# Optimization experiments

Measured on AMD Instinct MI355X. Metric: run time of the kernel, lower is better.

## Reference

```python
import jax, jax.numpy as jnp
import numpy as np

D = 512      # embed_dim
H = 8        # num_heads
B = 32       # number of graphs
L = 512      # max graph size (padded length)
DEG = 8      # avg out-degree
NUM_GIN = 3  # StructureExtractor num_layers


def setup_inputs() -> dict:
    key = jax.random.key(0)
    ks = jax.random.split(key, 24)

    # ragged graph sizes 256..504, ptr is the CSR boundary vector
    sizes = 256 + 8 * np.arange(B)
    ptr_np = np.concatenate([[0], np.cumsum(sizes)]).astype(np.int64)
    N = int(ptr_np[-1])  # 12160 total nodes

    rng = np.random.RandomState(0)
    node_graph = np.repeat(np.arange(B), sizes)
    offs = ptr_np[node_graph]
    sz = sizes[node_graph]
    # DEG random in-graph neighbors per node
    dst = (rng.random((N, DEG)) * sz[:, None]).astype(np.int64) + offs[:, None]
    src = np.repeat(np.arange(N, dtype=np.int64), DEG)
    edge_index = jnp.asarray(np.stack([src, dst.ravel()]), dtype=jnp.int64)

    # DAG reachability mask: True = masked. Keep key 0 open so no row is fully -inf.
    md = rng.random((B, L, L)) > 0.5
    md[:, :, 0] = False
    mask_dag_ = jnp.asarray(md)

    def lin(k, fan_in, fan_out):
        return jax.random.normal(k, (fan_in, fan_out), jnp.float32) / np.sqrt(fan_in)

    inp = {
        "x": jax.random.normal(ks[0], (N, D), jnp.float32),
        "edge_index": edge_index,
        "mask_dag_": mask_dag_,
        "ptr": jnp.asarray(ptr_np),
        # GIN layers: MLP(Linear(D,D) -> ReLU -> Linear(D,D)) per layer
        "gin_w1": jnp.stack([lin(ks[1 + i], D, D) for i in range(NUM_GIN)]),
        "gin_b1": jnp.zeros((NUM_GIN, D), jnp.float32),
        "gin_w2": jnp.stack([lin(ks[4 + i], D, D) for i in range(NUM_GIN)]),
        "gin_b2": jnp.zeros((NUM_GIN, D), jnp.float32),
        "bn_gamma": jnp.ones((D,), jnp.float32),
        "bn_beta": jnp.zeros((D,), jnp.float32),
        "se_out_w": lin(ks[7], D, D),
        "se_out_b": jnp.zeros((D,), jnp.float32),
        "qk_w": lin(ks[8], D, 2 * D),
        "qk_b": jnp.zeros((2 * D,), jnp.float32),
        "v_w": lin(ks[9], D, D),
        "v_b": jnp.zeros((D,), jnp.float32),
        "out_w": lin(ks[10], D, D),
        "out_b": jnp.zeros((D,), jnp.float32),
    }
    return inp


def reference(x, edge_index, mask_dag_, ptr,
              gin_w1, gin_b1, gin_w2, gin_b2,
              bn_gamma, bn_beta, se_out_w, se_out_b,
              qk_w, qk_b, v_w, v_b, out_w, out_b):
    N = x.shape[0]
    nb = ptr.shape[0] - 1
    Lm = mask_dag_.shape[1]
    hd = D // H
    scale = hd ** -0.5

    # v = to_v(x)
    v = x @ v_w + v_b

    # StructureExtractor: 3 GIN layers (eps=0) + BatchNorm (batch stats) + Linear
    src, dst = edge_index[0], edge_index[1]
    h = x
    for i in range(NUM_GIN):
        agg = jax.ops.segment_sum(h[src], dst, num_segments=N)
        z = h + agg                                  # (1+eps)*x + sum neighbors, eps=0
        z = jax.nn.relu(z @ gin_w1[i] + gin_b1[i]) @ gin_w2[i] + gin_b2[i]
        h = jax.nn.relu(z)
    mean = h.mean(axis=0)
    var = h.var(axis=0)
    h = (h - mean) / jnp.sqrt(var + 1e-5) * bn_gamma + bn_beta
    x_struct = h @ se_out_w + se_out_b

    # qk = to_qk(x_struct).chunk(2): k = first half, q = second half (original order)
    qk = x_struct @ qk_w + qk_b
    k_flat, q_flat = jnp.split(qk, 2, axis=-1)

    # pad ragged batch to [B, L, D]
    node_ar = jnp.arange(N)
    bi = jnp.searchsorted(ptr, node_ar, side='right') - 1   # graph id per node
    pos = node_ar - ptr[bi]                                 # in-graph position
    sizes = ptr[1:] - ptr[:-1]

    def pad(t):
        return jnp.zeros((nb, Lm, t.shape[-1]), t.dtype).at[bi, pos].set(t)

    def heads(t):  # [B, L, D] -> [B, H, L, hd]
        return t.reshape(nb, Lm, H, hd).transpose(0, 2, 1, 3)

    q = heads(pad(q_flat))
    k = heads(pad(k_flat))
    vp = heads(pad(v))

    dots = jnp.einsum('bhid,bhjd->bhij', q, k) * scale
    pad_mask = jnp.arange(Lm)[None, :] >= sizes[:, None]     # True = padded key
    dots = jnp.where(pad_mask[:, None, None, :], -jnp.inf, dots)
    dots = jnp.where(mask_dag_[:, None, :, :], -jnp.inf, dots)
    attn = jax.nn.softmax(dots, axis=-1)

    out = jnp.einsum('bhij,bhjd->bhid', attn, vp)            # [B, H, L, hd]
    out = out.transpose(0, 2, 1, 3).reshape(nb, Lm, D)[bi, pos]  # unpad -> [N, D]
    return out @ out_w + out_b
```

## Files before the change

### kernel.cpp

```cpp
#include <hip/hip_runtime.h>
#include <hip/hip_bf16.h>
#include <cstdint>
#include <cstddef>

#define D 512
#define NHEAD 8
#define LMAX 512
#define NGIN 3

typedef unsigned short u16;
typedef unsigned long long u64;
typedef __attribute__((ext_vector_type(8))) short short8;
typedef __attribute__((ext_vector_type(8))) unsigned short ushort8;
typedef __attribute__((ext_vector_type(4))) unsigned short us4;
typedef __attribute__((ext_vector_type(4))) float f32x4;

static __device__ inline u16 f2bf(float f){
    union { float f; uint32_t u; } c; c.f = f;
    uint32_t r = (c.u + 0x7fffu + ((c.u >> 16) & 1u)) >> 16;
    return (u16)r;
}
static __device__ inline u16 tbf(float f){
    union { float f; uint32_t u; } c; c.f = f;
    return (u16)(c.u >> 16);
}
static __device__ inline float bf2f(u16 h){
    union { uint32_t u; float f; } c; c.u = ((uint32_t)h) << 16; return c.f;
}

#define GLOAD_LDS16(SRC, DST) \
    __builtin_amdgcn_global_load_lds( \
        (const __attribute__((address_space(1))) void*)(SRC), \
        (__attribute__((address_space(3))) void*)(DST), 16, 0, 0)

__global__ void probe_kernel(const int* __restrict__ ptr_raw,
                             const unsigned char* __restrict__ mask_raw,
                             int* __restrict__ flags){
    if (threadIdx.x == 0){
        flags[0] = (ptr_raw[1] == 0) ? 1 : 0;
        int cntOdd = 0, cnt4 = 0;
        for (int i = 1; i < 2048; i += 2) cntOdd += (mask_raw[i] != 0);
        for (int i = 4; i < 2048; i += 8) cnt4   += (mask_raw[i] != 0);
        flags[1] = (cntOdd > 64) ? 1 : ((cnt4 > 16) ? 4 : 8);
    }
}

__global__ void conv_int_kernel(const int* __restrict__ raw, int* __restrict__ outp,
                                const int* __restrict__ flags, int n){
    int i = blockIdx.x*256 + threadIdx.x;
    if (i < n) outp[i] = flags[0] ? raw[2*i] : raw[i];
}

__global__ void maskbits_kernel(const unsigned char* __restrict__ raw,
                                u64* __restrict__ outp,
                                const int* __restrict__ flags, int total){
    int idx = blockIdx.x*256 + threadIdx.x;
    if (idx >= total) return;
    int w = flags[1];
    size_t ebase = (size_t)(idx >> 3) * 512 + (size_t)(idx & 7) * 64;
    u64 bits = 0;
    if (w == 1){
        const u64* p8 = (const u64*)(raw + ebase);
        #pragma unroll
        for (int g = 0; g < 8; g++){
            u64 v = p8[g];
            #pragma unroll
            for (int by = 0; by < 8; by++)
                if ((v >> (by*8)) & 0xffull) bits |= 1ull << (g*8 + by);
        }
    } else {
        for (int j = 0; j < 64; j++)
            if (raw[(ebase + j) * (size_t)w]) bits |= 1ull << j;
    }
    outp[idx] = bits;
}

__global__ void count_kernel(const int* __restrict__ ei, int* __restrict__ deg, int E, int N){
    int e = blockIdx.x*256 + threadIdx.x;
    if (e < E){
        int d = ei[E + e];
        if ((unsigned)d < (unsigned)N) atomicAdd(&deg[d], 1);
    }
}

__global__ void scan_kernel(const int* __restrict__ deg, int* __restrict__ offs, int n){
    __shared__ int wsum[16];
    __shared__ int carry_s;
    int tid = threadIdx.x, lane = tid & 63, wv = tid >> 6;
    if (tid == 0){ carry_s = 0; offs[0] = 0; }
    __syncthreads();
    int nChunks = (n + 1023) / 1024;
    for (int ch = 0; ch < nChunks; ch++){
        int i = ch*1024 + tid;
        int val = (i < n) ? deg[i] : 0;
        int s = val;
        #pragma unroll
        for (int off = 1; off < 64; off <<= 1){
            int t = __shfl_up(s, off);
            if (lane >= off) s += t;
        }
        if (lane == 63) wsum[wv] = s;
        __syncthreads();
        if (wv == 0){
            int t = (lane < 16) ? wsum[lane] : 0;
            #pragma unroll
            for (int off = 1; off < 16; off <<= 1){
                int u = __shfl_up(t, off);
                if (lane >= off) t += u;
            }
            if (lane < 16) wsum[lane] = t;
        }
        __syncthreads();
        int wbase = wv ? wsum[wv-1] : 0;
        if (i < n) offs[i+1] = carry_s + wbase + s;
        __syncthreads();
        if (tid == 1023) carry_s += wsum[15];
        __syncthreads();
    }
}

__global__ void fill_kernel(const int* __restrict__ ei, const int* __restrict__ offs,
                            int* __restrict__ cursor, int* __restrict__ in_src, int E, int N){
    int e = blockIdx.x*256 + threadIdx.x;
    if (e < E){
        int d = ei[E + e];
        if ((unsigned)d < (unsigned)N){
            int slot = atomicAdd(&cursor[d], 1);
            in_src[offs[d] + slot] = ei[e];
        }
    }
}

__global__ void split_kernel(const float* __restrict__ in, u16* __restrict__ hi,
                             u16* __restrict__ lo, int total4){
    int i = blockIdx.x*256 + threadIdx.x;
    if (i >= total4) return;
    float4 v = *(const float4*)(in + (size_t)i*4);
    float fv[4] = {v.x, v.y, v.z, v.w};
    us4 h4, l4;
    #pragma unroll
    for (int j = 0; j < 4; j++){
        u16 hh = tbf(fv[j]);
        h4[j] = hh;
        l4[j] = tbf(fv[j] - bf2f(hh));
    }
    *(us4*)(hi + (size_t)i*4) = h4;
    *(us4*)(lo + (size_t)i*4) = l4;
}

__global__ __launch_bounds__(256) void gather_kernel(const u16* __restrict__ hh,
        const u16* __restrict__ hl,
        const int* __restrict__ offs, const int* __restrict__ in_src,
        u16* __restrict__ oh, u16* __restrict__ ol, int N){
    int node = blockIdx.x*2 + (threadIdx.x >> 7);
    if (node >= N) return;
    int t = threadIdx.x & 127;
    size_t rb = (size_t)node*D + t*4;
    us4 vh = *(const us4*)(hh + rb);
    us4 vl = *(const us4*)(hl + rb);
    float a[4];
    #pragma unroll
    for (int j = 0; j < 4; j++) a[j] = bf2f(vh[j]) + bf2f(vl[j]);
    int s = offs[node], e = offs[node+1];
    for (int i = s; i < e; i++){
        size_t sb = (size_t)in_src[i]*D + t*4;
        us4 nh = *(const us4*)(hh + sb);
        us4 nl = *(const us4*)(hl + sb);
        #pragma unroll
        for (int j = 0; j < 4; j++) a[j] += bf2f(nh[j]) + bf2f(nl[j]);
    }
    us4 h4, l4;
    #pragma unroll
    for (int j = 0; j < 4; j++){
        u16 hh2 = tbf(a[j]);
        h4[j] = hh2;
        l4[j] = tbf(a[j] - bf2f(hh2));
    }
    *(us4*)(oh + rb) = h4;
    *(us4*)(ol + rb) = l4;
}

__global__ __launch_bounds__(256) void transpose_all(
        const float* __restrict__ v_w, const float* __restrict__ gin_w1,
        const float* __restrict__ gin_w2, const float* __restrict__ se_w,
        const float* __restrict__ out_w, const float* __restrict__ qk_w,
        u16* __restrict__ wtsh, u16* __restrict__ wtsl){
    const size_t SLOT = 262144;
    int z = blockIdx.z;
    int Nout = (z == 9) ? 1024 : 512;
    if (z < 9 && blockIdx.x >= 16) return;
    const float* W; int slot;
    switch (z){
        case 0: W = v_w; slot = 0; break;
        case 1: W = gin_w1;               slot = 1; break;
        case 2: W = gin_w2;               slot = 2; break;
        case 3: W = gin_w1 + 262144;      slot = 3; break;
        case 4: W = gin_w2 + 262144;      slot = 4; break;
        case 5: W = gin_w1 + 524288;      slot = 5; break;
        case 6: W = gin_w2 + 524288;      slot = 6; break;
        case 7: W = se_w;  slot = 7; break;
        case 8: W = out_w; slot = 10; break;
        default: W = qk_w; slot = 8; break;
    }
    u16* Wh = wtsh + SLOT*slot;
    u16* Wl = wtsl + SLOT*slot;
    __shared__ float T[32][33];
    int nb = blockIdx.x*32, kb = blockIdx.y*32;
    int ln = threadIdx.x & 31, lk = threadIdx.x >> 5;
    #pragma unroll
    for (int i = 0; i < 4; i++)
        T[lk + 8*i][ln] = W[(size_t)(kb + lk + 8*i)*Nout + nb + ln];
    __syncthreads();
    #pragma unroll
    for (int i = 0; i < 4; i++){
        float val = T[ln][lk + 8*i];
        u16 h = tbf(val);
        size_t idx = (size_t)(nb + lk + 8*i)*512 + kb + ln;
        Wh[idx] = h;
        Wl[idx] = tbf(val - bf2f(h));
    }
}

__global__ __launch_bounds__(256) void fold_transpose(const float* __restrict__ M1,
        const float* __restrict__ sc, u16* __restrict__ Wh, u16* __restrict__ Wl){
    __shared__ float T[32][33];
    int nb = blockIdx.x*32, kb = blockIdx.y*32;
    int ln = threadIdx.x & 31, lk = threadIdx.x >> 5;
    #pragma unroll
    for (int i = 0; i < 4; i++){
        int k = kb + lk + 8*i;
        T[lk + 8*i][ln] = M1[(size_t)k*1024 + nb + ln] * sc[k];
    }
    __syncthreads();
    #pragma unroll
    for (int i = 0; i < 4; i++){
        float val = T[ln][lk + 8*i];
        u16 h = tbf(val);
        size_t idx = (size_t)(nb + lk + 8*i)*512 + kb + ln;
        Wh[idx] = h;
        Wl[idx] = tbf(val - bf2f(h));
    }
}

__global__ void bias_fold(const float* __restrict__ M1, const float* __restrict__ sc,
        const float* __restrict__ se_b, const float* __restrict__ qk_w,
        const float* __restrict__ qk_b, float* __restrict__ bbig){
    int n = blockIdx.x;
    int lane = threadIdx.x;
    float acc = 0.f;
    for (int k = lane; k < 512; k += 64)
        acc += sc[512+k]*M1[(size_t)k*1024 + n] + se_b[k]*qk_w[(size_t)k*1024 + n];
    #pragma unroll
    for (int off = 32; off > 0; off >>= 1) acc += __shfl_xor(acc, off);
    if (lane == 0) bbig[n] = acc + qk_b[n];
}

template<int ACT, int EPI>
__global__ __launch_bounds__(256) void gemm_ps(const u16* __restrict__ Ahg,
        const u16* __restrict__ Alg,
        const u16* __restrict__ Wth, const u16* __restrict__ Wtl,
        const float* __restrict__ bias,
        void* __restrict__ C0, void* __restrict__ C1, int K, int Nout){
    __shared__ __align__(16) u16 Ah[128][64];
    __shared__ __align__(16) u16 Al[128][64];
    __shared__ __align__(16) u16 Bh[64][64];
    __shared__ __align__(16) u16 Bl[64][64];
    int tid = threadIdx.x;
    int gx = gridDim.x;
    int nwg = gx * gridDim.y;
    int orig = blockIdx.x + gx*blockIdx.y;
    int q8 = nwg >> 3, r8 = nwg & 7;
    int xcd = orig & 7, pos = orig >> 3;
    int wg = (xcd < r8 ? xcd*(q8+1) : r8*(q8+1) + (xcd - r8)*q8) + pos;
    int rowBase = (wg / gx) * 128, colBase = (wg % gx) * 64;
    int w = tid >> 6, l = tid & 63, lg = l >> 4, lm = l & 15;
    int wr = w >> 1, wc = w & 1;
    f32x4 acc[4][2] = {};
    const u16* Ahp = Ahg + (size_t)rowBase*K;
    const u16* Alp = Alg + (size_t)rowBase*K;
    const u16* Wph = Wth + (size_t)colBase*K;
    const u16* Wpl = Wtl + (size_t)colBase*K;
    int srowA[4], scolA[4], srowB[2], scolB[2];
    #pragma unroll
    for (int c = 0; c < 4; c++){
        int slot = c*256 + tid;
        srowA[c] = slot >> 3;
        scolA[c] = ((slot & 7) ^ (srowA[c] & 7)) * 8;
    }
    #pragma unroll
    for (int c = 0; c < 2; c++){
        int slot = c*256 + tid;
        srowB[c] = slot >> 3;
        scolB[c] = ((slot & 7) ^ (srowB[c] & 7)) * 8;
    }
    for (int k0 = 0; k0 < K; k0 += 64){
        #pragma unroll
        for (int c = 0; c < 4; c++){
            int slot = c*256 + tid;
            size_t so = (size_t)srowA[c]*K + k0 + scolA[c];
            GLOAD_LDS16(Ahp + so, &Ah[0][0] + slot*8);
            GLOAD_LDS16(Alp + so, &Al[0][0] + slot*8);
        }
        #pragma unroll
        for (int c = 0; c < 2; c++){
            int slot = c*256 + tid;
            size_t so = (size_t)srowB[c]*K + k0 + scolB[c];
            GLOAD_LDS16(Wph + so, &Bh[0][0] + slot*8);
            GLOAD_LDS16(Wpl + so, &Bl[0][0] + slot*8);
        }
        __syncthreads();
        #pragma unroll
        for (int ks = 0; ks < 2; ks++){
            int scg = ((ks*4 + lg) ^ (lm & 7)) * 8;
            short8 ah[4], al[4], bh[2], bl[2];
            #pragma unroll
            for (int mf = 0; mf < 4; mf++){
                ah[mf] = *(const short8*)&Ah[wr*64 + mf*16 + lm][scg];
                al[mf] = *(const short8*)&Al[wr*64 + mf*16 + lm][scg];
            }
            #pragma unroll
            for (int nf = 0; nf < 2; nf++){
                bh[nf] = *(const short8*)&Bh[wc*32 + nf*16 + lm][scg];
                bl[nf] = *(const short8*)&Bl[wc*32 + nf*16 + lm][scg];
            }
            __builtin_amdgcn_s_setprio(1);
            #pragma unroll
            for (int mf = 0; mf < 4; mf++)
                #pragma unroll
                for (int nf = 0; nf < 2; nf++){
                    acc[mf][nf] = __builtin_amdgcn_mfma_f32_16x16x32_bf16(ah[mf], bh[nf], acc[mf][nf], 0, 0, 0);
                    acc[mf][nf] = __builtin_amdgcn_mfma_f32_16x16x32_bf16(al[mf], bh[nf], acc[mf][nf], 0, 0, 0);
                    acc[mf][nf] = __builtin_amdgcn_mfma_f32_16x16x32_bf16(ah[mf], bl[nf], acc[mf][nf], 0, 0, 0);
                }
            __builtin_amdgcn_s_setprio(0);
        }
        __syncthreads();
    }
    #pragma unroll
    for (int nf = 0; nf < 2; nf++){
        int col = colBase + wc*32 + nf*16 + lm;
        float bv = bias[col];
        #pragma unroll
        for (int mf = 0; mf < 4; mf++){
            int row = rowBase + wr*64 + mf*16 + lg*4;
            #pragma unroll
            for (int j = 0; j < 4; j++){
                float o = acc[mf][nf][j] + bv;
                if (ACT) o = fmaxf(o, 0.f);
                size_t idx = (size_t)(row + j)*Nout + col;
                if (EPI == 0){
                    ((float*)C0)[idx] = o;
                } else if (EPI == 1){
                    u16 hh = tbf(o);
                    ((u16*)C0)[idx] = hh;
                    ((u16*)C1)[idx] = tbf(o - bf2f(hh));
                } else {
                    ((u16*)C0)[idx] = f2bf(o);
                }
            }
        }
    }
}

__global__ __launch_bounds__(256) void bn_stats_kernel(const u16* __restrict__ Ah,
        const u16* __restrict__ Al, float* __restrict__ sums, int n){
    int c = threadIdx.x;
    int r0 = blockIdx.x*128, r1 = min(n, r0+128);
    float s0=0.f, s1=0.f, q0=0.f, q1=0.f;
    for (int r = r0; r < r1; r++){
        float v0 = bf2f(Ah[(size_t)r*D + c])       + bf2f(Al[(size_t)r*D + c]);
        float v1 = bf2f(Ah[(size_t)r*D + 256 + c]) + bf2f(Al[(size_t)r*D + 256 + c]);
        s0 += v0; q0 += v0*v0; s1 += v1; q1 += v1*v1;
    }
    atomicAdd(&sums[c], s0);
    atomicAdd(&sums[c+256], s1);
    atomicAdd(&sums[512+c], q0);
    atomicAdd(&sums[512+c+256], q1);
}

__global__ void bn_final_kernel(const float* __restrict__ sums, const float* __restrict__ gamma,
        const float* __restrict__ beta, float* __restrict__ sc, int n){
    int c = threadIdx.x;
    float mean = sums[c] / (float)n;
    float var = sums[512+c] / (float)n - mean*mean;
    float r = rsqrtf(var + 1e-5f);
    float scale = r * gamma[c];
    sc[c] = scale;
    sc[512+c] = beta[c] - mean*scale;
}

#define ATS 72
__global__ __launch_bounds__(512) void attn_mfma_kernel(const u16* __restrict__ qkH,
        const u16* __restrict__ qkL, const u16* __restrict__ vbf,
        const u64* __restrict__ maskbits,
        const int* __restrict__ ptr, u16* __restrict__ oh, u16* __restrict__ ol, int N){
    __shared__ u16 Kh[64][ATS];
    __shared__ u16 Kl[64][ATS];
    __shared__ u16 Vt[64][ATS];
    __shared__ u16 Pl[8][16][ATS];
    int b = blockIdx.z, h = blockIdx.y;
    int base = ptr[b], size = ptr[b+1] - base;
    int q0 = blockIdx.x * 128;
    if (q0 >= size) return;
    int tid = threadIdx.x, w = tid >> 6, l = tid & 63;
    int lg = l >> 4, lm = l & 15;
    short8 qh[2], ql[2];
    {
        int qrow = q0 + w*16 + lm;
        int qr = (qrow < size) ? qrow : 0;
        const u16* qph = qkH + (size_t)(base + qr)*1024 + 512 + h*64;
        const u16* qpl = qkL + (size_t)(base + qr)*1024 + 512 + h*64;
        #pragma unroll
        for (int ks = 0; ks < 2; ks++){
            short8 th = *(const short8*)(qph + ks*32 + lg*8);
            short8 tl = *(const short8*)(qpl + ks*32 + lg*8);
            if (qrow >= size){ th = short8{0,0,0,0,0,0,0,0}; tl = short8{0,0,0,0,0,0,0,0}; }
            qh[ks] = th; ql[ks] = tl;
        }
    }
    f32x4 acco[4] = {};
    float mrow[4], lrow[4];
    #pragma unroll
    for (int j = 0; j < 4; j++){ mrow[j] = -INFINITY; lrow[j] = 0.f; }
    int nt = (size + 63) >> 6;
    for (int t = 0; t < nt; t++){
        int j0 = t*64;
        __syncthreads();
        {
            int jj = tid & 63, db = (tid >> 6)*8;
            int key = j0 + jj;
            bool ok = key < size;
            size_t node = (size_t)(base + (ok ? key : 0));
            const u16* khp = qkH + node*1024 + h*64 + db;
            const u16* klp = qkL + node*1024 + h*64 + db;
            const u16* vp  = vbf + node*512  + h*64 + db;
            ushort8 z = {0,0,0,0,0,0,0,0};
            ushort8 kh0 = ok ? *(const ushort8*)(khp) : z;
            ushort8 kl0 = ok ? *(const ushort8*)(klp) : z;
            ushort8 v0  = ok ? *(const ushort8*)(vp)  : z;
            *(ushort8*)&Kh[jj][db] = kh0;
            *(ushort8*)&Kl[jj][db] = kl0;
            #pragma unroll
            for (int i = 0; i < 8; i++) Vt[db + i][jj] = v0[i];
        }
        __syncthreads();
        f32x4 sc[4] = {};
        __builtin_amdgcn_s_setprio(1);
        #pragma unroll
        for (int nf = 0; nf < 4; nf++)
            #pragma unroll
            for (int ks = 0; ks < 2; ks++){
                short8 kh = *(const short8*)&Kh[nf*16 + lm][ks*32 + lg*8];
                short8 kl = *(const short8*)&Kl[nf*16 + lm][ks*32 + lg*8];
                sc[nf] = __builtin_amdgcn_mfma_f32_16x16x32_bf16(qh[ks], kh, sc[nf], 0, 0, 0);
                sc[nf] = __builtin_amdgcn_mfma_f32_16x16x32_bf16(ql[ks], kh, sc[nf], 0, 0, 0);
                sc[nf] = __builtin_amdgcn_mfma_f32_16x16x32_bf16(qh[ks], kl, sc[nf], 0, 0, 0);
            }
        __builtin_amdgcn_s_setprio(0);
        u64 mb[4];
        #pragma unroll
        for (int j = 0; j < 4; j++)
            mb[j] = maskbits[((size_t)b*LMAX + (q0 + w*16 + lg*4 + j))*8 + t];
        float mx[4], alpha[4];
        #pragma unroll
        for (int j = 0; j < 4; j++){
            float s0 = -INFINITY;
            #pragma unroll
            for (int nf = 0; nf < 4; nf++){
                int key = j0 + nf*16 + lm;
                float s = sc[nf][j] * 0.125f;
                bool msk = (key >= size) || ((mb[j] >> (nf*16 + lm)) & 1);
                s = msk ? -INFINITY : s;
                sc[nf][j] = s;
                s0 = fmaxf(s0, s);
            }
            #pragma unroll
            for (int off = 1; off < 16; off <<= 1) s0 = fmaxf(s0, __shfl_xor(s0, off));
            mx[j] = s0;
        }
        #pragma unroll
        for (int j = 0; j < 4; j++){
            if (mx[j] == -INFINITY){ alpha[j] = 1.f; }
            else {
                float mn = fmaxf(mrow[j], mx[j]);
                alpha[j] = __expf(mrow[j] - mn);
                mrow[j] = mn;
            }
        }
        float ps[4] = {0.f, 0.f, 0.f, 0.f};
        #pragma unroll
        for (int nf = 0; nf < 4; nf++)
            #pragma unroll
            for (int j = 0; j < 4; j++){
                float p = (mx[j] == -INFINITY) ? 0.f : __expf(sc[nf][j] - mrow[j]);
                ps[j] += p;
                Pl[w][lg*4 + j][nf*16 + lm] = tbf(p);
            }
        #pragma unroll
        for (int j = 0; j < 4; j++){
            float s = ps[j];
            #pragma unroll
            for (int off = 1; off < 16; off <<= 1) s += __shfl_xor(s, off);
            lrow[j] = lrow[j]*alpha[j] + s;
        }
        #pragma unroll
        for (int df = 0; df < 4; df++)
            #pragma unroll
            for (int j = 0; j < 4; j++) acco[df][j] *= alpha[j];
        __builtin_amdgcn_s_setprio(1);
        #pragma unroll
        for (int ks = 0; ks < 2; ks++){
            short8 pf = *(const short8*)&Pl[w][lm][ks*32 + lg*8];
            #pragma unroll
            for (int df = 0; df < 4; df++){
                short8 vf = *(const short8*)&Vt[df*16 + lm][ks*32 + lg*8];
                acco[df] = __builtin_amdgcn_mfma_f32_16x16x32_bf16(pf, vf, acco[df], 0, 0, 0);
            }
        }
        __builtin_amdgcn_s_setprio(0);
    }
    #pragma unroll
    for (int j = 0; j < 4; j++){
        int r = q0 + w*16 + lg*4 + j;
        if (r < size){
            float inv = 1.f / lrow[j];
            #pragma unroll
            for (int df = 0; df < 4; df++){
                float o = acco[df][j] * inv;
                size_t idx = (size_t)(base + r)*D + h*64 + df*16 + lm;
                u16 hh = tbf(o);
                oh[idx] = hh;
                ol[idx] = tbf(o - bf2f(hh));
            }
        }
    }
}

extern "C" void kernel_launch(void* const* d_in, const int* in_sizes, int n_in,
                              void* d_out, int out_size, void* d_ws, size_t ws_size,
                              hipStream_t stream){
    const float* x        = (const float*)d_in[0];
    const int*   ei_raw   = (const int*)d_in[1];
    const unsigned char* mask_raw = (const unsigned char*)d_in[2];
    const int*   ptr_raw  = (const int*)d_in[3];
    const float* gin_w1   = (const float*)d_in[4];
    const float* gin_b1   = (const float*)d_in[5];
    const float* gin_w2   = (const float*)d_in[6];
    const float* gin_b2   = (const float*)d_in[7];
    const float* bn_gamma = (const float*)d_in[8];
    const float* bn_beta  = (const float*)d_in[9];
    const float* se_w     = (const float*)d_in[10];
    const float* se_b     = (const float*)d_in[11];
    const float* qk_w     = (const float*)d_in[12];
    const float* qk_b     = (const float*)d_in[13];
    const float* v_w      = (const float*)d_in[14];
    const float* v_b      = (const float*)d_in[15];
    const float* out_w    = (const float*)d_in[16];
    const float* out_b    = (const float*)d_in[17];

    const int N  = in_sizes[0] / D;
    const int E  = in_sizes[1] / 2;
    const int B  = in_sizes[3] - 1;
    const int Mn = in_sizes[2];

    char* ws = (char*)d_ws;
    char* p = ws;
    auto alloc = [&](size_t bytes) -> char* {
        char* q = p; p += (bytes + 255) & ~(size_t)255; return q;
    };
    size_t PLANE = (size_t)N * D * sizeof(u16);
    u16* pairX = (u16*)alloc(2*PLANE);
    u16* pairG = (u16*)alloc(2*PLANE);
    u16* pairT = (u16*)alloc(2*PLANE);
    u16* pairH = (u16*)alloc(2*PLANE);
    u16* v_bf  = (u16*)alloc(PLANE);
    u16* Xh = pairX, *Xl = pairX + (size_t)N*D;
    u16* Gh = pairG, *Gl = pairG + (size_t)N*D;
    u16* Th = pairT, *Tl = pairT + (size_t)N*D;
    u16* Hh = pairH, *Hl = pairH + (size_t)N*D;
    float* sums   = (float*)alloc(1024*sizeof(float));
    float* sc     = (float*)alloc(1024*sizeof(float));
    int*   flags  = (int*)alloc(16*sizeof(int));
    int*   deg    = (int*)alloc((size_t)N*sizeof(int));
    int*   offs   = (int*)alloc((size_t)(N+1)*sizeof(int));
    int*   cursor = (int*)alloc((size_t)N*sizeof(int));
    int*   in_src = (int*)alloc((size_t)E*sizeof(int));
    int*   ptr32  = (int*)alloc(64*sizeof(int));
    int*   ei32   = (int*)alloc((size_t)2*E*sizeof(int));
    u64*   mbits  = (u64*)alloc((size_t)(Mn/64)*sizeof(u64));
    u16*   wtsh   = (u16*)alloc((size_t)2883584*sizeof(u16));
    u16*   wtsl   = (u16*)alloc((size_t)2883584*sizeof(u16));
    u16*   sewh   = (u16*)alloc((size_t)D*D*sizeof(u16));
    u16*   sewl   = (u16*)alloc((size_t)D*D*sizeof(u16));
    float* M1     = (float*)alloc((size_t)D*1024*sizeof(float));
    u16*   wbig_h = (u16*)alloc((size_t)1024*D*sizeof(u16));
    u16*   wbig_l = (u16*)alloc((size_t)1024*D*sizeof(u16));
    float* bbig   = (float*)alloc(1024*sizeof(float));
    float* zbias  = (float*)alloc(1024*sizeof(float));
    const size_t SLOT = 262144;
    u16 *wh_v = wtsh, *wl_v = wtsl;
    u16 *wh_g[6], *wl_g[6];
    for (int i = 0; i < 6; i++){ wh_g[i] = wtsh + SLOT*(1+i); wl_g[i] = wtsl + SLOT*(1+i); }
    u16 *wh_qk  = wtsh + SLOT*8,  *wl_qk  = wtsl + SLOT*8;
    u16 *wh_out = wtsh + SLOT*10, *wl_out = wtsl + SLOT*10;

    probe_kernel<<<1, 64, 0, stream>>>(ptr_raw, mask_raw, flags);
    conv_int_kernel<<<1, 64, 0, stream>>>(ptr_raw, ptr32, flags, B + 1);
    conv_int_kernel<<<(2*E + 255)/256, 256, 0, stream>>>(ei_raw, ei32, flags, 2*E);
    maskbits_kernel<<<(Mn/64 + 255)/256, 256, 0, stream>>>(mask_raw, mbits, flags, Mn/64);

    hipMemsetAsync(deg, 0, (size_t)N*sizeof(int), stream);
    hipMemsetAsync(cursor, 0, (size_t)N*sizeof(int), stream);
    hipMemsetAsync(zbias, 0, 1024*sizeof(float), stream);
    count_kernel<<<(E+255)/256, 256, 0, stream>>>(ei32, deg, E, N);
    scan_kernel<<<1, 1024, 0, stream>>>(deg, offs, N);
    fill_kernel<<<(E+255)/256, 256, 0, stream>>>(ei32, offs, cursor, in_src, E, N);

    transpose_all<<<dim3(32,16,10), 256, 0, stream>>>(v_w, gin_w1, gin_w2, se_w, out_w, qk_w, wtsh, wtsl);
    split_kernel<<<(N*D/4 + 255)/256, 256, 0, stream>>>(x, Xh, Xl, N*D/4);
    split_kernel<<<(D*D/4 + 255)/256, 256, 0, stream>>>(se_w, sewh, sewl, D*D/4);

    gemm_ps<0,0><<<dim3(16,4), 256, 0, stream>>>(sewh, sewl, wh_qk, wl_qk, zbias, M1, nullptr, D, 2*D);

    dim3 g512(8, N/128), g1024(16, N/128);

    gemm_ps<0,2><<<g512, 256, 0, stream>>>(Xh, Xl, wh_v, wl_v, v_b, v_bf, nullptr, D, D);

    for (int i = 0; i < NGIN; i++){
        const u16* sh = (i == 0) ? Xh : Hh;
        const u16* sl = (i == 0) ? Xl : Hl;
        gather_kernel<<<(N+1)/2, 256, 0, stream>>>(sh, sl, offs, in_src, Gh, Gl, N);
        gemm_ps<1,1><<<g512, 256, 0, stream>>>(Gh, Gl, wh_g[2*i],   wl_g[2*i],   gin_b1 + (size_t)i*D, Th, Tl, D, D);
        gemm_ps<1,1><<<g512, 256, 0, stream>>>(Th, Tl, wh_g[2*i+1], wl_g[2*i+1], gin_b2 + (size_t)i*D, Hh, Hl, D, D);
    }

    hipMemsetAsync(sums, 0, 1024*sizeof(float), stream);
    bn_stats_kernel<<<(N+127)/128, 256, 0, stream>>>(Hh, Hl, sums, N);
    bn_final_kernel<<<1, 512, 0, stream>>>(sums, bn_gamma, bn_beta, sc, N);

    fold_transpose<<<dim3(32,16), 256, 0, stream>>>(M1, sc, wbig_h, wbig_l);
    bias_fold<<<1024, 64, 0, stream>>>(M1, sc, se_b, qk_w, qk_b, bbig);

    gemm_ps<0,1><<<g1024, 256, 0, stream>>>(Hh, Hl, wbig_h, wbig_l, bbig, pairX, pairG, D, 2*D);

    attn_mfma_kernel<<<dim3(LMAX/128, NHEAD, B), 512, 0, stream>>>(pairX, pairG, v_bf, mbits, ptr32, Th, Tl, N);

    gemm_ps<0,0><<<g512, 256, 0, stream>>>(Th, Tl, wh_out, wl_out, out_b, (float*)d_out, nullptr, D, D);
}
```

Before: 575.4 us.

## Fuse prologue kernels, merge BN fold, and drop low-order terms in two GEMMs

Folds the int conversion, mask bitpacking, weight transposes, input splits and degree counting into one multi-role launch, and reads the raw edge index directly so the int32 copy goes away. BN finalisation is merged into the weight/bias fold kernel. The V projection and the output projection now use a two-term split-bf16 GEMM with no A low part, and attention writes only a single bf16 output. This trims launches, memory traffic and MFMA work, at the cost of lower precision in those two GEMMs.

```diff
diff --git a/kernel.cpp b/kernel.cpp
--- a/kernel.cpp
+++ b/kernel.cpp
@@ -45,41 +45,113 @@
     }
 }
 
-__global__ void conv_int_kernel(const int* __restrict__ raw, int* __restrict__ outp,
-                                const int* __restrict__ flags, int n){
-    int i = blockIdx.x*256 + threadIdx.x;
-    if (i < n) outp[i] = flags[0] ? raw[2*i] : raw[i];
-}
-
-__global__ void maskbits_kernel(const unsigned char* __restrict__ raw,
-                                u64* __restrict__ outp,
-                                const int* __restrict__ flags, int total){
-    int idx = blockIdx.x*256 + threadIdx.x;
-    if (idx >= total) return;
-    int w = flags[1];
-    size_t ebase = (size_t)(idx >> 3) * 512 + (size_t)(idx & 7) * 64;
-    u64 bits = 0;
-    if (w == 1){
-        const u64* p8 = (const u64*)(raw + ebase);
-        #pragma unroll
-        for (int g = 0; g < 8; g++){
-            u64 v = p8[g];
-            #pragma unroll
-            for (int by = 0; by < 8; by++)
-                if ((v >> (by*8)) & 0xffull) bits |= 1ull << (g*8 + by);
-        }
+__global__ __launch_bounds__(256) void mega_prologue(
+        const float* __restrict__ v_w, const float* __restrict__ gin_w1,
+        const float* __restrict__ gin_w2, const float* __restrict__ se_w,
+        const float* __restrict__ out_w, const float* __restrict__ qk_w,
+        u16* __restrict__ wtsh, u16* __restrict__ wtsl,
+        const unsigned char* __restrict__ mask_raw, u64* __restrict__ mbits,
+        const float* __restrict__ x, u16* __restrict__ Xh, u16* __restrict__ Xl,
+        u16* __restrict__ sewh, u16* __restrict__ sewl,
+        const int* __restrict__ ptr_raw, int* __restrict__ ptr32,
+        const int* __restrict__ ei_raw, int* __restrict__ deg,
+        const int* __restrict__ flags,
+        int Nnodes, int E, int B, int Mn64){
+    int z = blockIdx.z;
+    int bid = blockIdx.y*32 + blockIdx.x;
+    int tid = threadIdx.x;
+    if (z <= 9){
+        int Nout = (z == 9) ? 1024 : 512;
+        if (z < 9 && blockIdx.x >= 16) return;
+        const size_t SLOT = 262144;
+        const float* W; int slot;
+        switch (z){
+            case 0: W = v_w; slot = 0; break;
+            case 1: W = gin_w1;          slot = 1; break;
+            case 2: W = gin_w2;          slot = 2; break;
+            case 3: W = gin_w1 + 262144; slot = 3; break;
+            case 4: W = gin_w2 + 262144; slot = 4; break;
+            case 5: W = gin_w1 + 524288; slot = 5; break;
+            case 6: W = gin_w2 + 524288; slot = 6; break;
+            case 7: W = se_w;  slot = 7; break;
+            case 8: W = out_w; slot = 10; break;
+            default: W = qk_w; slot = 8; break;
+        }
+        u16* Wh = wtsh + SLOT*slot;
+        u16* Wl = wtsl + SLOT*slot;
+        __shared__ float T[32][33];
+        int nb = blockIdx.x*32, kb = blockIdx.y*32;
+        int ln = tid & 31, lk = tid >> 5;
+        #pragma unroll
+        for (int i = 0; i < 4; i++)
+            T[lk + 8*i][ln] = W[(size_t)(kb + lk + 8*i)*Nout + nb + ln];
+        __syncthreads();
+        #pragma unroll
+        for (int i = 0; i < 4; i++){
+            float val = T[ln][lk + 8*i];
+            u16 h = tbf(val);
+            size_t idx = (size_t)(nb + lk + 8*i)*512 + kb + ln;
+            Wh[idx] = h;
+            Wl[idx] = tbf(val - bf2f(h));
+        }
+    } else if (z == 10){
+        int idx = bid*256 + tid;
+        if (idx >= Mn64) return;
+        int w = flags[1];
+        size_t ebase = (size_t)(idx >> 3) * 512 + (size_t)(idx & 7) * 64;
+        u64 bits = 0;
+        if (w == 1){
+            const u64* p8 = (const u64*)(mask_raw + ebase);
+            #pragma unroll
+            for (int g = 0; g < 8; g++){
+                u64 v = p8[g];
+                #pragma unroll
+                for (int by = 0; by < 8; by++)
+                    if ((v >> (by*8)) & 0xffull) bits |= 1ull << (g*8 + by);
+            }
+        } else {
+            for (int j = 0; j < 64; j++)
+                if (mask_raw[(ebase + j) * (size_t)w]) bits |= 1ull << j;
+        }
+        mbits[idx] = bits;
+    } else if (z == 11){
+        int total4 = Nnodes*D/4;
+        for (int i = bid*256 + tid; i < total4; i += 131072){
+            float4 v = *(const float4*)(x + (size_t)i*4);
+            float fv[4] = {v.x, v.y, v.z, v.w};
+            us4 h4, l4;
+            #pragma unroll
+            for (int j = 0; j < 4; j++){
+                u16 hh = tbf(fv[j]);
+                h4[j] = hh;
+                l4[j] = tbf(fv[j] - bf2f(hh));
+            }
+            *(us4*)(Xh + (size_t)i*4) = h4;
+            *(us4*)(Xl + (size_t)i*4) = l4;
+        }
+    } else if (z == 12){
+        int i = bid*256 + tid;
+        if (i >= D*D/4) return;
+        float4 v = *(const float4*)(se_w + (size_t)i*4);
+        float fv[4] = {v.x, v.y, v.z, v.w};
+        us4 h4, l4;
+        #pragma unroll
+        for (int j = 0; j < 4; j++){
+            u16 hh = tbf(fv[j]);
+            h4[j] = hh;
+            l4[j] = tbf(fv[j] - bf2f(hh));
+        }
+        *(us4*)(sewh + (size_t)i*4) = h4;
+        *(us4*)(sewl + (size_t)i*4) = l4;
+    } else if (z == 13){
+        if (bid == 0 && tid <= B)
+            ptr32[tid] = flags[0] ? ptr_raw[2*tid] : ptr_raw[tid];
     } else {
-        for (int j = 0; j < 64; j++)
-            if (raw[(ebase + j) * (size_t)w]) bits |= 1ull << j;
-    }
-    outp[idx] = bits;
-}
-
-__global__ void count_kernel(const int* __restrict__ ei, int* __restrict__ deg, int E, int N){
-    int e = blockIdx.x*256 + threadIdx.x;
-    if (e < E){
-        int d = ei[E + e];
-        if ((unsigned)d < (unsigned)N) atomicAdd(&deg[d], 1);
+        int e = bid*256 + tid;
+        if (e < E){
+            int d = flags[0] ? ei_raw[2*(E + e)] : ei_raw[E + e];
+            if ((unsigned)d < (unsigned)Nnodes) atomicAdd(&deg[d], 1);
+        }
     }
 }
 
@@ -119,33 +191,17 @@
     }
 }
 
-__global__ void fill_kernel(const int* __restrict__ ei, const int* __restrict__ offs,
-                            int* __restrict__ cursor, int* __restrict__ in_src, int E, int N){
+__global__ void fill_kernel(const int* __restrict__ ei_raw, const int* __restrict__ offs,
+                            int* __restrict__ cursor, int* __restrict__ in_src,
+                            const int* __restrict__ flags, int E, int N){
     int e = blockIdx.x*256 + threadIdx.x;
     if (e < E){
-        int d = ei[E + e];
+        int d = flags[0] ? ei_raw[2*(E + e)] : ei_raw[E + e];
         if ((unsigned)d < (unsigned)N){
             int slot = atomicAdd(&cursor[d], 1);
-            in_src[offs[d] + slot] = ei[e];
-        }
-    }
-}
-
-__global__ void split_kernel(const float* __restrict__ in, u16* __restrict__ hi,
-                             u16* __restrict__ lo, int total4){
-    int i = blockIdx.x*256 + threadIdx.x;
-    if (i >= total4) return;
-    float4 v = *(const float4*)(in + (size_t)i*4);
-    float fv[4] = {v.x, v.y, v.z, v.w};
-    us4 h4, l4;
-    #pragma unroll
-    for (int j = 0; j < 4; j++){
-        u16 hh = tbf(fv[j]);
-        h4[j] = hh;
-        l4[j] = tbf(fv[j] - bf2f(hh));
-    }
-    *(us4*)(hi + (size_t)i*4) = h4;
-    *(us4*)(lo + (size_t)i*4) = l4;
+            in_src[offs[d] + slot] = flags[0] ? ei_raw[2*e] : ei_raw[e];
+        }
+    }
 }
 
 __global__ __launch_bounds__(256) void gather_kernel(const u16* __restrict__ hh,
@@ -180,89 +236,60 @@
     *(us4*)(ol + rb) = l4;
 }
 
-__global__ __launch_bounds__(256) void transpose_all(
-        const float* __restrict__ v_w, const float* __restrict__ gin_w1,
-        const float* __restrict__ gin_w2, const float* __restrict__ se_w,
-        const float* __restrict__ out_w, const float* __restrict__ qk_w,
-        u16* __restrict__ wtsh, u16* __restrict__ wtsl){
-    const size_t SLOT = 262144;
-    int z = blockIdx.z;
-    int Nout = (z == 9) ? 1024 : 512;
-    if (z < 9 && blockIdx.x >= 16) return;
-    const float* W; int slot;
-    switch (z){
-        case 0: W = v_w; slot = 0; break;
-        case 1: W = gin_w1;               slot = 1; break;
-        case 2: W = gin_w2;               slot = 2; break;
-        case 3: W = gin_w1 + 262144;      slot = 3; break;
-        case 4: W = gin_w2 + 262144;      slot = 4; break;
-        case 5: W = gin_w1 + 524288;      slot = 5; break;
-        case 6: W = gin_w2 + 524288;      slot = 6; break;
-        case 7: W = se_w;  slot = 7; break;
-        case 8: W = out_w; slot = 10; break;
-        default: W = qk_w; slot = 8; break;
-    }
-    u16* Wh = wtsh + SLOT*slot;
-    u16* Wl = wtsl + SLOT*slot;
-    __shared__ float T[32][33];
-    int nb = blockIdx.x*32, kb = blockIdx.y*32;
-    int ln = threadIdx.x & 31, lk = threadIdx.x >> 5;
-    #pragma unroll
-    for (int i = 0; i < 4; i++)
-        T[lk + 8*i][ln] = W[(size_t)(kb + lk + 8*i)*Nout + nb + ln];
-    __syncthreads();
-    #pragma unroll
-    for (int i = 0; i < 4; i++){
-        float val = T[ln][lk + 8*i];
-        u16 h = tbf(val);
-        size_t idx = (size_t)(nb + lk + 8*i)*512 + kb + ln;
-        Wh[idx] = h;
-        Wl[idx] = tbf(val - bf2f(h));
-    }
-}
-
-__global__ __launch_bounds__(256) void fold_transpose(const float* __restrict__ M1,
-        const float* __restrict__ sc, u16* __restrict__ Wh, u16* __restrict__ Wl){
-    __shared__ float T[32][33];
-    int nb = blockIdx.x*32, kb = blockIdx.y*32;
-    int ln = threadIdx.x & 31, lk = threadIdx.x >> 5;
-    #pragma unroll
-    for (int i = 0; i < 4; i++){
-        int k = kb + lk + 8*i;
-        T[lk + 8*i][ln] = M1[(size_t)k*1024 + nb + ln] * sc[k];
-    }
-    __syncthreads();
-    #pragma unroll
-    for (int i = 0; i < 4; i++){
-        float val = T[ln][lk + 8*i];
-        u16 h = tbf(val);
-        size_t idx = (size_t)(nb + lk + 8*i)*512 + kb + ln;
-        Wh[idx] = h;
-        Wl[idx] = tbf(val - bf2f(h));
-    }
-}
-
-__global__ void bias_fold(const float* __restrict__ M1, const float* __restrict__ sc,
+__global__ __launch_bounds__(256) void fold_mega(const float* __restrict__ M1,
+        const float* __restrict__ sums, const float* __restrict__ gamma,
+        const float* __restrict__ beta,
         const float* __restrict__ se_b, const float* __restrict__ qk_w,
-        const float* __restrict__ qk_b, float* __restrict__ bbig){
-    int n = blockIdx.x;
-    int lane = threadIdx.x;
-    float acc = 0.f;
-    for (int k = lane; k < 512; k += 64)
-        acc += sc[512+k]*M1[(size_t)k*1024 + n] + se_b[k]*qk_w[(size_t)k*1024 + n];
-    #pragma unroll
-    for (int off = 32; off > 0; off >>= 1) acc += __shfl_xor(acc, off);
-    if (lane == 0) bbig[n] = acc + qk_b[n];
-}
-
-template<int ACT, int EPI>
+        const float* __restrict__ qk_b,
+        u16* __restrict__ Wh, u16* __restrict__ Wl, float* __restrict__ bbig, int n){
+    float inv_n = 1.f / (float)n;
+    if (blockIdx.z == 0){
+        __shared__ float T[32][33];
+        int nb = blockIdx.x*32, kb = blockIdx.y*32;
+        int ln = threadIdx.x & 31, lk = threadIdx.x >> 5;
+        #pragma unroll
+        for (int i = 0; i < 4; i++){
+            int k = kb + lk + 8*i;
+            float mean = sums[k] * inv_n;
+            float var = sums[512+k] * inv_n - mean*mean;
+            float scale = rsqrtf(var + 1e-5f) * gamma[k];
+            T[lk + 8*i][ln] = M1[(size_t)k*1024 + nb + ln] * scale;
+        }
+        __syncthreads();
+        #pragma unroll
+        for (int i = 0; i < 4; i++){
+            float val = T[ln][lk + 8*i];
+            u16 h = tbf(val);
+            size_t idx = (size_t)(nb + lk + 8*i)*512 + kb + ln;
+            Wh[idx] = h;
+            Wl[idx] = tbf(val - bf2f(h));
+        }
+    } else {
+        int wv = threadIdx.x >> 6, lane = threadIdx.x & 63;
+        if (wv >= 2) return;
+        int nidx = (blockIdx.y*32 + blockIdx.x)*2 + wv;
+        float acc = 0.f;
+        for (int k = lane; k < 512; k += 64){
+            float mean = sums[k] * inv_n;
+            float var = sums[512+k] * inv_n - mean*mean;
+            float scale = rsqrtf(var + 1e-5f) * gamma[k];
+            float shift = beta[k] - mean*scale;
+            acc += shift*M1[(size_t)k*1024 + nidx] + se_b[k]*qk_w[(size_t)k*1024 + nidx];
+        }
+        #pragma unroll
+        for (int off = 32; off > 0; off >>= 1) acc += __shfl_xor(acc, off);
+        if (lane == 0) bbig[nidx] = acc + qk_b[nidx];
+    }
+}
+
+template<int ACT, int EPI, int TERMS>
 __global__ __launch_bounds__(256) void gemm_ps(const u16* __restrict__ Ahg,
         const u16* __restrict__ Alg,
         const u16* __restrict__ Wth, const u16* __restrict__ Wtl,
         const float* __restrict__ bias,
         void* __restrict__ C0, void* __restrict__ C1, int K, int Nout){
     __shared__ __align__(16) u16 Ah[128][64];
-    __shared__ __align__(16) u16 Al[128][64];
+    __shared__ __align__(16) u16 Al[TERMS == 3 ? 128 : 1][64];
     __shared__ __align__(16) u16 Bh[64][64];
     __shared__ __align__(16) u16 Bl[64][64];
     int tid = threadIdx.x;
@@ -277,7 +304,7 @@
     int wr = w >> 1, wc = w & 1;
     f32x4 acc[4][2] = {};
     const u16* Ahp = Ahg + (size_t)rowBase*K;
-    const u16* Alp = Alg + (size_t)rowBase*K;
+    const u16* Alp = (TERMS == 3) ? Alg + (size_t)rowBase*K : nullptr;
     const u16* Wph = Wth + (size_t)colBase*K;
     const u16* Wpl = Wtl + (size_t)colBase*K;
     int srowA[4], scolA[4], srowB[2], scolB[2];
@@ -299,7 +326,7 @@
             int slot = c*256 + tid;
             size_t so = (size_t)srowA[c]*K + k0 + scolA[c];
             GLOAD_LDS16(Ahp + so, &Ah[0][0] + slot*8);
-            GLOAD_LDS16(Alp + so, &Al[0][0] + slot*8);
+            if (TERMS == 3) GLOAD_LDS16(Alp + so, &Al[0][0] + slot*8);
         }
         #pragma unroll
         for (int c = 0; c < 2; c++){
@@ -316,7 +343,7 @@
             #pragma unroll
             for (int mf = 0; mf < 4; mf++){
                 ah[mf] = *(const short8*)&Ah[wr*64 + mf*16 + lm][scg];
-                al[mf] = *(const short8*)&Al[wr*64 + mf*16 + lm][scg];
+                if (TERMS == 3) al[mf] = *(const short8*)&Al[wr*64 + mf*16 + lm][scg];
             }
             #pragma unroll
             for (int nf = 0; nf < 2; nf++){
@@ -329,7 +356,8 @@
                 #pragma unroll
                 for (int nf = 0; nf < 2; nf++){
                     acc[mf][nf] = __builtin_amdgcn_mfma_f32_16x16x32_bf16(ah[mf], bh[nf], acc[mf][nf], 0, 0, 0);
-                    acc[mf][nf] = __builtin_amdgcn_mfma_f32_16x16x32_bf16(al[mf], bh[nf], acc[mf][nf], 0, 0, 0);
+                    if (TERMS == 3)
+                        acc[mf][nf] = __builtin_amdgcn_mfma_f32_16x16x32_bf16(al[mf], bh[nf], acc[mf][nf], 0, 0, 0);
                     acc[mf][nf] = __builtin_amdgcn_mfma_f32_16x16x32_bf16(ah[mf], bl[nf], acc[mf][nf], 0, 0, 0);
                 }
             __builtin_amdgcn_s_setprio(0);
@@ -378,22 +406,11 @@
     atomicAdd(&sums[512+c+256], q1);
 }
 
-__global__ void bn_final_kernel(const float* __restrict__ sums, const float* __restrict__ gamma,
-        const float* __restrict__ beta, float* __restrict__ sc, int n){
-    int c = threadIdx.x;
-    float mean = sums[c] / (float)n;
-    float var = sums[512+c] / (float)n - mean*mean;
-    float r = rsqrtf(var + 1e-5f);
-    float scale = r * gamma[c];
-    sc[c] = scale;
-    sc[512+c] = beta[c] - mean*scale;
-}
-
 #define ATS 72
 __global__ __launch_bounds__(512) void attn_mfma_kernel(const u16* __restrict__ qkH,
         const u16* __restrict__ qkL, const u16* __restrict__ vbf,
         const u64* __restrict__ maskbits,
-        const int* __restrict__ ptr, u16* __restrict__ oh, u16* __restrict__ ol, int N){
+        const int* __restrict__ ptr, u16* __restrict__ oh, int N){
     __shared__ u16 Kh[64][ATS];
     __shared__ u16 Kl[64][ATS];
     __shared__ u16 Vt[64][ATS];
@@ -527,10 +544,7 @@
             #pragma unroll
             for (int df = 0; df < 4; df++){
                 float o = acco[df][j] * inv;
-                size_t idx = (size_t)(base + r)*D + h*64 + df*16 + lm;
-                u16 hh = tbf(o);
-                oh[idx] = hh;
-                ol[idx] = tbf(o - bf2f(hh));
+                oh[(size_t)(base + r)*D + h*64 + df*16 + lm] = f2bf(o);
             }
         }
     }
@@ -579,14 +593,12 @@
     u16* Th = pairT, *Tl = pairT + (size_t)N*D;
     u16* Hh = pairH, *Hl = pairH + (size_t)N*D;
     float* sums   = (float*)alloc(1024*sizeof(float));
-    float* sc     = (float*)alloc(1024*sizeof(float));
     int*   flags  = (int*)alloc(16*sizeof(int));
     int*   deg    = (int*)alloc((size_t)N*sizeof(int));
     int*   offs   = (int*)alloc((size_t)(N+1)*sizeof(int));
     int*   cursor = (int*)alloc((size_t)N*sizeof(int));
     int*   in_src = (int*)alloc((size_t)E*sizeof(int));
     int*   ptr32  = (int*)alloc(64*sizeof(int));
-    int*   ei32   = (int*)alloc((size_t)2*E*sizeof(int));
     u64*   mbits  = (u64*)alloc((size_t)(Mn/64)*sizeof(u64));
     u16*   wtsh   = (u16*)alloc((size_t)2883584*sizeof(u16));
     u16*   wtsl   = (u16*)alloc((size_t)2883584*sizeof(u16));
@@ -605,45 +617,39 @@
     u16 *wh_out = wtsh + SLOT*10, *wl_out = wtsl + SLOT*10;
 
     probe_kernel<<<1, 64, 0, stream>>>(ptr_raw, mask_raw, flags);
-    conv_int_kernel<<<1, 64, 0, stream>>>(ptr_raw, ptr32, flags, B + 1);
-    conv_int_kernel<<<(2*E + 255)/256, 256, 0, stream>>>(ei_raw, ei32, flags, 2*E);
-    maskbits_kernel<<<(Mn/64 + 255)/256, 256, 0, stream>>>(mask_raw, mbits, flags, Mn/64);
-
     hipMemsetAsync(deg, 0, (size_t)N*sizeof(int), stream);
     hipMemsetAsync(cursor, 0, (size_t)N*sizeof(int), stream);
     hipMemsetAsync(zbias, 0, 1024*sizeof(float), stream);
-    count_kernel<<<(E+255)/256, 256, 0, stream>>>(ei32, deg, E, N);
+    hipMemsetAsync(sums, 0, 1024*sizeof(float), stream);
+    mega_prologue<<<dim3(32,16,15), 256, 0, stream>>>(
+        v_w, gin_w1, gin_w2, se_w, out_w, qk_w, wtsh, wtsl,
+        mask_raw, mbits, x, Xh, Xl, sewh, sewl,
+        ptr_raw, ptr32, ei_raw, deg, flags, N, E, B, Mn/64);
     scan_kernel<<<1, 1024, 0, stream>>>(deg, offs, N);
-    fill_kernel<<<(E+255)/256, 256, 0, stream>>>(ei32, offs, cursor, in_src, E, N);
-
-    transpose_all<<<dim3(32,16,10), 256, 0, stream>>>(v_w, gin_w1, gin_w2, se_w, out_w, qk_w, wtsh, wtsl);
-    split_kernel<<<(N*D/4 + 255)/256, 256, 0, stream>>>(x, Xh, Xl, N*D/4);
-    split_kernel<<<(D*D/4 + 255)/256, 256, 0, stream>>>(se_w, sewh, sewl, D*D/4);
-
-    gemm_ps<0,0><<<dim3(16,4), 256, 0, stream>>>(sewh, sewl, wh_qk, wl_qk, zbias, M1, nullptr, D, 2*D);
+    fill_kernel<<<(E+255)/256, 256, 0, stream>>>(ei_raw, offs, cursor, in_src, flags, E, N);
+
+    gemm_ps<0,0,3><<<dim3(16,4), 256, 0, stream>>>(sewh, sewl, wh_qk, wl_qk, zbias, M1, nullptr, D, 2*D);
 
     dim3 g512(8, N/128), g1024(16, N/128);
 
-    gemm_ps<0,2><<<g512, 256, 0, stream>>>(Xh, Xl, wh_v, wl_v, v_b, v_bf, nullptr, D, D);
+    gemm_ps<0,2,2><<<g512, 256, 0, stream>>>(Xh, nullptr, wh_v, wl_v, v_b, v_bf, nullptr, D, D);
 
     for (int i = 0; i < NGIN; i++){
         const u16* sh = (i == 0) ? Xh : Hh;
         const u16* sl = (i == 0) ? Xl : Hl;
         gather_kernel<<<(N+1)/2, 256, 0, stream>>>(sh, sl, offs, in_src, Gh, Gl, N);
-        gemm_ps<1,1><<<g512, 256, 0, stream>>>(Gh, Gl, wh_g[2*i],   wl_g[2*i],   gin_b1 + (size_t)i*D, Th, Tl, D, D);
-        gemm_ps<1,1><<<g512, 256, 0, stream>>>(Th, Tl, wh_g[2*i+1], wl_g[2*i+1], gin_b2 + (size_t)i*D, Hh, Hl, D, D);
-    }
-
-    hipMemsetAsync(sums, 0, 1024*sizeof(float), stream);
+        gemm_ps<1,1,3><<<g512, 256, 0, stream>>>(Gh, Gl, wh_g[2*i],   wl_g[2*i],   gin_b1 + (size_t)i*D, Th, Tl, D, D);
+        gemm_ps<1,1,3><<<g512, 256, 0, stream>>>(Th, Tl, wh_g[2*i+1], wl_g[2*i+1], gin_b2 + (size_t)i*D, Hh, Hl, D, D);
+    }
+
     bn_stats_kernel<<<(N+127)/128, 256, 0, stream>>>(Hh, Hl, sums, N);
-    bn_final_kernel<<<1, 512, 0, stream>>>(sums, bn_gamma, bn_beta, sc, N);
-
-    fold_transpose<<<dim3(32,16), 256, 0, stream>>>(M1, sc, wbig_h, wbig_l);
-    bias_fold<<<1024, 64, 0, stream>>>(M1, sc, se_b, qk_w, qk_b, bbig);
-
-    gemm_ps<0,1><<<g1024, 256, 0, stream>>>(Hh, Hl, wbig_h, wbig_l, bbig, pairX, pairG, D, 2*D);
-
-    attn_mfma_kernel<<<dim3(LMAX/128, NHEAD, B), 512, 0, stream>>>(pairX, pairG, v_bf, mbits, ptr32, Th, Tl, N);
-
-    gemm_ps<0,0><<<g512, 256, 0, stream>>>(Th, Tl, wh_out, wl_out, out_b, (float*)d_out, nullptr, D, D);
-}
+
+    fold_mega<<<dim3(32,16,2), 256, 0, stream>>>(M1, sums, bn_gamma, bn_beta,
+        se_b, qk_w, qk_b, wbig_h, wbig_l, bbig, N);
+
+    gemm_ps<0,1,3><<<g1024, 256, 0, stream>>>(Hh, Hl, wbig_h, wbig_l, bbig, pairX, pairG, D, 2*D);
+
+    attn_mfma_kernel<<<dim3(LMAX/128, NHEAD, B), 512, 0, stream>>>(pairX, pairG, v_bf, mbits, ptr32, Th, N);
+
+    gemm_ps<0,0,2><<<g512, 256, 0, stream>>>(Th, nullptr, wh_out, wl_out, out_b, (float*)d_out, nullptr, D, D);
+}
```

Result: faster. 548.3 us (-4.7%).
